# Kernel tuning notes

Measured on AMD Instinct MI355X. Metric: run time of the kernel, lower is better.

The kernel has to match this reference:

```python
import jax, jax.numpy as jnp
import numpy as np

SEQ, B, IN, H = 256, 64, 512, 1024


def setup_inputs() -> dict:
    key = jax.random.key(0)
    ks = jax.random.split(key, 17)
    s_in = 0.05  # small init to avoid gate saturation
    inp = {"x": jax.random.normal(ks[0], (SEQ, B, IN), dtype=jnp.float32)}
    names = ["f", "i", "o", "c"]
    for j, g in enumerate(names):
        inp[f"W_i{g}"] = jax.random.normal(ks[1 + 4 * j], (H, IN), dtype=jnp.float32) * s_in
        inp[f"b_i{g}"] = jax.random.normal(ks[2 + 4 * j], (H,), dtype=jnp.float32) * s_in
        inp[f"W_h{g}"] = jax.random.normal(ks[3 + 4 * j], (H, H), dtype=jnp.float32) * s_in
        inp[f"b_h{g}"] = jax.random.normal(ks[4 + 4 * j], (H,), dtype=jnp.float32) * s_in
    return inp


def reference(x, W_if, b_if, W_hf, b_hf, W_ii, b_ii, W_hi, b_hi,
              W_io, b_io, W_ho, b_ho, W_ic, b_ic, W_hc, b_hc):
    # Precompute input-to-gate projections for the whole sequence (one big GEMM each)
    xf = jnp.einsum('sbi,hi->sbh', x, W_if) + b_if
    xi = jnp.einsum('sbi,hi->sbh', x, W_ii) + b_ii
    xo = jnp.einsum('sbi,hi->sbh', x, W_io) + b_io
    xc = jnp.einsum('sbi,hi->sbh', x, W_ic) + b_ic

    batch = x.shape[1]
    hidden = W_hf.shape[0]
    h0 = jnp.zeros((batch, hidden), dtype=x.dtype)
    c0 = jnp.zeros((batch, hidden), dtype=x.dtype)

    def step(carry, xs):
        h, c = carry
        xf_t, xi_t, xo_t, xc_t = xs
        f = jax.nn.sigmoid(xf_t + h @ W_hf.T + b_hf)
        i = jax.nn.sigmoid(xi_t + h @ W_hi.T + b_hi)
        o = jax.nn.sigmoid(xo_t + h @ W_ho.T + b_ho)
        g = jnp.tanh(xc_t + h @ W_hc.T + b_hc)
        c_new = f * c + i * g
        h_new = o * jnp.tanh(c_new)
        return (h_new, c_new), h_new

    (h_fin, c_fin), h_seq = jax.lax.scan(step, (h0, c0), (xf, xi, xo, xc))
    # match torch module's (1, B, H) leading layer dim on final states
    return h_seq, h_fin[None], c_fin[None]
```

## Files before the change

kernel.cpp:

```cpp
#include <hip/hip_runtime.h>
#include <hip/hip_bf16.h>

typedef __bf16 bf16_t;
typedef __bf16 bf16x8 __attribute__((ext_vector_type(8)));
typedef float f32x4 __attribute__((ext_vector_type(4)));
typedef int   i32x4 __attribute__((ext_vector_type(4)));

#define SEQLEN 256
#define NBATCH 64
#define INDIM  512
#define HID    1024
#define NBLK   256

#define XF_OFF   0ull
#define WXF_OFF  16777216ull
#define WHF_OFF  20971520ull
#define BS_OFF   29360128ull
#define HSEQ_OFF 29376512ull
#define FLG_OFF  63062016ull
#define SLOT_BYTES 131072ull
#define SLOT_ELEMS 65536

__device__ __forceinline__ bf16x8 cvt8(float4 a, float4 b) {
  bf16x8 v;
  v[0] = (bf16_t)a.x; v[1] = (bf16_t)a.y; v[2] = (bf16_t)a.z; v[3] = (bf16_t)a.w;
  v[4] = (bf16_t)b.x; v[5] = (bf16_t)b.y; v[6] = (bf16_t)b.z; v[7] = (bf16_t)b.w;
  return v;
}

__global__ __launch_bounds__(256) void pack_xf_k(const float* __restrict__ x,
                                                 bf16_t* __restrict__ xf) {
  int idx = blockIdx.x * 256 + threadIdx.x;
  int t = idx >> 12;
  int r = idx & 4095;
  int batch = r >> 6, c8 = r & 63;
  const float4* s = (const float4*)(x + ((size_t)t * NBATCH + batch) * INDIM + c8 * 8);
  int kk = c8 >> 2, lhi = c8 & 3;
  int kh = kk >> 3, kkl = kk & 7;
  int bg = batch >> 4, lane = (batch & 15) + 16 * lhi;
  bf16_t* d = xf + (size_t)t * 32768 + (size_t)(((bg * 2 + kh) * 8 + kkl) * 64 + lane) * 8;
  *(bf16x8*)d = cvt8(s[0], s[1]);
}

struct GatePtrs {
  const float* Wi[4];
  const float* bi[4];
  const float* Wh[4];
  const float* bh[4];
};

__global__ __launch_bounds__(256) void pack_w_k(GatePtrs p,
                                                bf16_t* __restrict__ Wxf,
                                                bf16_t* __restrict__ Whf,
                                                float* __restrict__ bsum) {
  int idx = blockIdx.x * 256 + threadIdx.x;
  int row = idx / 192;
  int c   = idx % 192;
  int blk = row >> 5, r32 = row & 31, g = r32 >> 3, jj = r32 & 7;
  int j = blk * 8 + jj;
  int g2 = r32 >> 4, lrow = r32 & 15;
  if (c == 0) bsum[row] = p.bi[g][j] + p.bh[g][j];
  if (c < 64) {
    const float4* s = (const float4*)(p.Wi[g] + (size_t)j * INDIM + c * 8);
    int kk = c >> 2, lane = lrow + 16 * (c & 3);
    *(bf16x8*)(Wxf + (size_t)blk * 16384 + (size_t)((kk * 2 + g2) * 64 + lane) * 8) = cvt8(s[0], s[1]);
  } else {
    int cc = c - 64;
    const float4* s = (const float4*)(p.Wh[g] + (size_t)j * HID + cc * 8);
    int kk = cc >> 2, lane = lrow + 16 * (cc & 3);
    *(bf16x8*)(Whf + (size_t)blk * 32768 + (size_t)((kk * 2 + g2) * 64 + lane) * 8) = cvt8(s[0], s[1]);
  }
}

__global__ __launch_bounds__(256) void finalize_k(const bf16_t* __restrict__ hseq,
                                                  float* __restrict__ out) {
  int idx = blockIdx.x * 256 + threadIdx.x;
  int c = idx & 127;
  int batch = (idx >> 7) & 63;
  int t = idx >> 13;
  int slot = (t < 256) ? (t + 1) : 256;
  int j0 = c * 8;
  int kkg = j0 >> 5;
  int sub = (j0 & 31) >> 3;
  int lane = (batch & 15) + 16 * sub;
  int bg2 = (batch >> 4) * 2 + (kkg >> 4);
  const bf16_t* src = hseq + (size_t)slot * SLOT_ELEMS + (size_t)((bg2 * 16 + (kkg & 15)) * 64 + lane) * 8;
  bf16x8 v = *(const bf16x8*)src;
  float* d = out + ((size_t)t * NBATCH + batch) * HID + j0;
  *(float4*)d       = make_float4((float)v[0], (float)v[1], (float)v[2], (float)v[3]);
  *(float4*)(d + 4) = make_float4((float)v[4], (float)v[5], (float)v[6], (float)v[7]);
}

#define PLDC(dst, ptr, OFF) \
  asm volatile("global_load_dwordx4 %0, %1, off offset:" OFF : "=v"(dst) : "v"(ptr))

__global__ __launch_bounds__(256, 1) void lstm_rec_k(const bf16_t* __restrict__ Whf,
                                                     const bf16_t* __restrict__ Wxf,
                                                     const bf16_t* __restrict__ xf,
                                                     const float* __restrict__ bsum,
                                                     bf16_t* __restrict__ hseq,
                                                     int* __restrict__ flags,
                                                     float* __restrict__ out) {
  const int b = blockIdx.x;
  const int cb = b & 127, bgs = b >> 7;
  const int tid = threadIdx.x;
  const int w = tid >> 6, l = tid & 63;
  const int bhalf = w >> 1, kh = w & 1;
  const int bg = bgs * 2 + bhalf;

  __shared__ bf16_t xwlds[16384];
  __shared__ float  accbuf[2][32][36];

#pragma unroll
  for (int i = 0; i < 8; ++i)
    __builtin_amdgcn_global_load_lds((const __attribute__((address_space(1))) void*)(Wxf + (size_t)cb * 16384 + (i * 256 + tid) * 8),
                                     (__attribute__((address_space(3))) void*)(xwlds + (i * 256 + tid) * 8),
                                     16, 0, 0);

  i32x4 whr[16][2];
  {
    const char* wb = (const char*)Whf + (size_t)cb * 65536 + (size_t)(kh * 32768) + (size_t)l * 16;
    const char* w0 = wb;          const char* w1 = wb + 4096;
    const char* w2 = wb + 8192;   const char* w3 = wb + 12288;
    const char* w4 = wb + 16384;  const char* w5 = wb + 20480;
    const char* w6 = wb + 24576;  const char* w7 = wb + 28672;
    PLDC(whr[0][0],  w0, "0"); PLDC(whr[0][1],  w0, "1024"); PLDC(whr[1][0],  w0, "2048"); PLDC(whr[1][1],  w0, "3072");
    PLDC(whr[2][0],  w1, "0"); PLDC(whr[2][1],  w1, "1024"); PLDC(whr[3][0],  w1, "2048"); PLDC(whr[3][1],  w1, "3072");
    PLDC(whr[4][0],  w2, "0"); PLDC(whr[4][1],  w2, "1024"); PLDC(whr[5][0],  w2, "2048"); PLDC(whr[5][1],  w2, "3072");
    PLDC(whr[6][0],  w3, "0"); PLDC(whr[6][1],  w3, "1024"); PLDC(whr[7][0],  w3, "2048"); PLDC(whr[7][1],  w3, "3072");
    PLDC(whr[8][0],  w4, "0"); PLDC(whr[8][1],  w4, "1024"); PLDC(whr[9][0],  w4, "2048"); PLDC(whr[9][1],  w4, "3072");
    PLDC(whr[10][0], w5, "0"); PLDC(whr[10][1], w5, "1024"); PLDC(whr[11][0], w5, "2048"); PLDC(whr[11][1], w5, "3072");
    PLDC(whr[12][0], w6, "0"); PLDC(whr[12][1], w6, "1024"); PLDC(whr[13][0], w6, "2048"); PLDC(whr[13][1], w6, "3072");
    PLDC(whr[14][0], w7, "0"); PLDC(whr[14][1], w7, "1024"); PLDC(whr[15][0], w7, "2048"); PLDC(whr[15][1], w7, "3072");
  }
  asm volatile("s_waitcnt vmcnt(0)" ::: "memory");
  __builtin_amdgcn_sched_barrier(0);

  const int eb = tid >> 3, ejj = tid & 7;
  const int gb = bgs * 32 + eb;
  const int j  = cb * 8 + ejj;
  const int p_lane = (gb & 15) + 16 * ((j & 31) >> 3);
  const int p_kkg = j >> 5;
  const size_t pub_off = (size_t)((((gb >> 4) * 2 + (p_kkg >> 4)) * 16 + (p_kkg & 15)) * 64 + p_lane) * 16
                       + (size_t)(j & 7) * 2;
  const float bsF = bsum[cb * 32 + ejj];
  const float bsI = bsum[cb * 32 + 8 + ejj];
  const float bsO = bsum[cb * 32 + 16 + ejj];
  const float bsC = bsum[cb * 32 + 24 + ejj];
  float cs = 0.f;

  const size_t pollbase = (size_t)((bg * 2 + kh) * 16) * 1024 + (size_t)l * 16;
  const char* fbase = (const char*)flags + (size_t)l * 16;

  __syncthreads();

  for (int t = 0; t < SEQLEN; ++t) {
    const char* xp0 = (const char*)xf + (size_t)t * 65536 + (size_t)((bg * 2 + kh) * 8 * 64 + l) * 16;
    const char* xp1 = xp0 + 4096;
    i32x4 xr[8];
    PLDC(xr[0], xp0, "0"); PLDC(xr[1], xp0, "1024"); PLDC(xr[2], xp0, "2048"); PLDC(xr[3], xp0, "3072");
    PLDC(xr[4], xp1, "0"); PLDC(xr[5], xp1, "1024"); PLDC(xr[6], xp1, "2048"); PLDC(xr[7], xp1, "3072");
    const char* fp = fbase + (size_t)t * 1024;
    i32x4 f;
    asm volatile("global_load_dwordx4 %0, %1, off sc0 sc1" : "=v"(f) : "v"(fp));

    asm volatile("s_waitcnt vmcnt(1)" ::: "memory");
    __builtin_amdgcn_sched_barrier(0);
    f32x4 acc0 = {}, acc1 = {};
#pragma unroll
    for (int kkl = 0; kkl < 8; ++kkl) {
      const int kk = kh * 8 + kkl;
      bf16x8 xv = __builtin_bit_cast(bf16x8, xr[kkl]);
      bf16x8 w0 = *(const bf16x8*)(xwlds + (size_t)((kk * 2 + 0) * 64 + l) * 8);
      bf16x8 w1 = *(const bf16x8*)(xwlds + (size_t)((kk * 2 + 1) * 64 + l) * 8);
      acc0 = __builtin_amdgcn_mfma_f32_16x16x32_bf16(xv, w0, acc0, 0, 0, 0);
      acc1 = __builtin_amdgcn_mfma_f32_16x16x32_bf16(xv, w1, acc1, 0, 0, 0);
    }

    asm volatile("s_waitcnt vmcnt(0)" ::: "memory");
    __builtin_amdgcn_sched_barrier(0);
    while (__any((f[0] == 0) | (f[1] == 0) | (f[2] == 0) | (f[3] == 0))) {
      __builtin_amdgcn_s_sleep(1);
      asm volatile("global_load_dwordx4 %0, %1, off sc0 sc1" : "=v"(f) : "v"(fp));
      asm volatile("s_waitcnt vmcnt(0)" ::: "memory");
      __builtin_amdgcn_sched_barrier(0);
    }

    const char* q0 = (const char*)hseq + (size_t)t * SLOT_BYTES + pollbase;
    const char* q1 = q0 + 4096;
    const char* q2 = q0 + 8192;
    const char* q3 = q0 + 12288;
    i32x4 hv[16];
    PLDC(hv[0],  q0, "0"); PLDC(hv[1],  q0, "1024"); PLDC(hv[2],  q0, "2048"); PLDC(hv[3],  q0, "3072");
    PLDC(hv[4],  q1, "0"); PLDC(hv[5],  q1, "1024"); PLDC(hv[6],  q1, "2048"); PLDC(hv[7],  q1, "3072");
    PLDC(hv[8],  q2, "0"); PLDC(hv[9],  q2, "1024"); PLDC(hv[10], q2, "2048"); PLDC(hv[11], q2, "3072");
    PLDC(hv[12], q3, "0"); PLDC(hv[13], q3, "1024"); PLDC(hv[14], q3, "2048"); PLDC(hv[15], q3, "3072");
    asm volatile("s_waitcnt vmcnt(0)" ::: "memory");
    __builtin_amdgcn_sched_barrier(0);

#pragma unroll
    for (int kkl = 0; kkl < 16; ++kkl) {
      bf16x8 hf = __builtin_bit_cast(bf16x8, hv[kkl]);
      acc0 = __builtin_amdgcn_mfma_f32_16x16x32_bf16(hf, __builtin_bit_cast(bf16x8, whr[kkl][0]), acc0, 0, 0, 0);
      acc1 = __builtin_amdgcn_mfma_f32_16x16x32_bf16(hf, __builtin_bit_cast(bf16x8, whr[kkl][1]), acc1, 0, 0, 0);
    }

    *(f32x4*)&accbuf[kh][l & 15][bhalf * 16 + (l >> 4) * 4]        = acc0;
    *(f32x4*)&accbuf[kh][16 + (l & 15)][bhalf * 16 + (l >> 4) * 4] = acc1;
    __syncthreads();

    {
      float pf = bsF + accbuf[0][ejj][eb]      + accbuf[1][ejj][eb];
      float pi = bsI + accbuf[0][8 + ejj][eb]  + accbuf[1][8 + ejj][eb];
      float po = bsO + accbuf[0][16 + ejj][eb] + accbuf[1][16 + ejj][eb];
      float pc = bsC + accbuf[0][24 + ejj][eb] + accbuf[1][24 + ejj][eb];
      float fg = 1.f / (1.f + __expf(-pf));
      float ig = 1.f / (1.f + __expf(-pi));
      float og = 1.f / (1.f + __expf(-po));
      float e2 = __expf(-2.f * fabsf(pc));
      float gg = __builtin_copysignf((1.f - e2) / (1.f + e2), pc);
      cs = fg * cs + ig * gg;
      float e2c = __expf(-2.f * fabsf(cs));
      float th = __builtin_copysignf((1.f - e2c) / (1.f + e2c), cs);
      float hval = og * th;

      unsigned int my = (unsigned int)__builtin_bit_cast(unsigned short, (bf16_t)hval);
      unsigned int other = __shfl_xor(my, 1);
      if (!(tid & 1)) {
        unsigned int pk = my | (other << 16);
        unsigned int* hd = (unsigned int*)((char*)hseq + (size_t)(t + 1) * SLOT_BYTES + pub_off);
        __hip_atomic_store(hd, pk, __ATOMIC_RELAXED, __HIP_MEMORY_SCOPE_AGENT);
      }
      if (t == SEQLEN - 1)
        out[(size_t)SEQLEN * NBATCH * HID + (size_t)NBATCH * HID + (size_t)gb * HID + j] = cs;
    }

    __syncthreads();
    if (t < SEQLEN - 1 && tid == 0)
      __hip_atomic_store(&flags[(t + 1) * NBLK + b], 1, __ATOMIC_RELAXED, __HIP_MEMORY_SCOPE_AGENT);
  }
}

extern "C" void kernel_launch(void* const* d_in, const int* in_sizes, int n_in,
                              void* d_out, int out_size, void* d_ws, size_t ws_size,
                              hipStream_t stream) {
  (void)in_sizes; (void)n_in; (void)out_size; (void)ws_size;
  char* ws = (char*)d_ws;
  bf16_t* xf   = (bf16_t*)(ws + XF_OFF);
  bf16_t* Wxf  = (bf16_t*)(ws + WXF_OFF);
  bf16_t* Whf  = (bf16_t*)(ws + WHF_OFF);
  float*  bs   = (float*)(ws + BS_OFF);
  bf16_t* hseq = (bf16_t*)(ws + HSEQ_OFF);
  int*    flg  = (int*)(ws + FLG_OFF);

  const float* x = (const float*)d_in[0];
  GatePtrs p;
  for (int g = 0; g < 4; ++g) {
    p.Wi[g] = (const float*)d_in[1 + 4 * g];
    p.bi[g] = (const float*)d_in[2 + 4 * g];
    p.Wh[g] = (const float*)d_in[3 + 4 * g];
    p.bh[g] = (const float*)d_in[4 + 4 * g];
  }

  pack_xf_k<<<4096, 256, 0, stream>>>(x, xf);
  pack_w_k<<<3072, 256, 0, stream>>>(p, Wxf, Whf, bs);
  hipMemsetAsync(flg, 1, NBLK * 4, stream);
  hipMemsetAsync(flg + NBLK, 0, 256 * NBLK * 4, stream);
  hipMemsetAsync(hseq, 0, SLOT_BYTES, stream);
  lstm_rec_k<<<NBLK, 256, 0, stream>>>(Whf, Wxf, xf, bs, hseq, flg, (float*)d_out);
  finalize_k<<<8224, 256, 0, stream>>>(hseq, (float*)d_out);
}
```

Before: 749.7 us.

## Restrict flag polling to batch-group peers and prefetch next step's x and flags

Each block now waits only on the flags of the 128 blocks in its own batch group, not on all 256 blocks. The next step's x tile and flag are loaded before the block barrier, and the flag is polled right after publishing, so the x projection MFMAs overlap the h loads. The accumulators are split into even and odd chains to break MFMA dependency chains. The s_sleep in the spin loop is removed, which cuts wake-up latency but adds more memory traffic while polling.

```diff
diff --git a/kernel.cpp b/kernel.cpp
--- a/kernel.cpp
+++ b/kernel.cpp
@@ -150,42 +150,30 @@
   float cs = 0.f;
 
   const size_t pollbase = (size_t)((bg * 2 + kh) * 16) * 1024 + (size_t)l * 16;
-  const char* fbase = (const char*)flags + (size_t)l * 16;
+  const char* fbase = (const char*)flags + (size_t)bgs * 512 + (size_t)(l & 31) * 16;
 
   __syncthreads();
 
-  for (int t = 0; t < SEQLEN; ++t) {
-    const char* xp0 = (const char*)xf + (size_t)t * 65536 + (size_t)((bg * 2 + kh) * 8 * 64 + l) * 16;
+  i32x4 xr[8];
+  {
+    const char* xp0 = (const char*)xf + (size_t)((bg * 2 + kh) * 8 * 64 + l) * 16;
     const char* xp1 = xp0 + 4096;
-    i32x4 xr[8];
     PLDC(xr[0], xp0, "0"); PLDC(xr[1], xp0, "1024"); PLDC(xr[2], xp0, "2048"); PLDC(xr[3], xp0, "3072");
     PLDC(xr[4], xp1, "0"); PLDC(xr[5], xp1, "1024"); PLDC(xr[6], xp1, "2048"); PLDC(xr[7], xp1, "3072");
-    const char* fp = fbase + (size_t)t * 1024;
+  }
+  {
     i32x4 f;
-    asm volatile("global_load_dwordx4 %0, %1, off sc0 sc1" : "=v"(f) : "v"(fp));
-
-    asm volatile("s_waitcnt vmcnt(1)" ::: "memory");
-    __builtin_amdgcn_sched_barrier(0);
-    f32x4 acc0 = {}, acc1 = {};
-#pragma unroll
-    for (int kkl = 0; kkl < 8; ++kkl) {
-      const int kk = kh * 8 + kkl;
-      bf16x8 xv = __builtin_bit_cast(bf16x8, xr[kkl]);
-      bf16x8 w0 = *(const bf16x8*)(xwlds + (size_t)((kk * 2 + 0) * 64 + l) * 8);
-      bf16x8 w1 = *(const bf16x8*)(xwlds + (size_t)((kk * 2 + 1) * 64 + l) * 8);
-      acc0 = __builtin_amdgcn_mfma_f32_16x16x32_bf16(xv, w0, acc0, 0, 0, 0);
-      acc1 = __builtin_amdgcn_mfma_f32_16x16x32_bf16(xv, w1, acc1, 0, 0, 0);
-    }
-
+    asm volatile("global_load_dwordx4 %0, %1, off sc0 sc1" : "=v"(f) : "v"(fbase));
     asm volatile("s_waitcnt vmcnt(0)" ::: "memory");
     __builtin_amdgcn_sched_barrier(0);
     while (__any((f[0] == 0) | (f[1] == 0) | (f[2] == 0) | (f[3] == 0))) {
-      __builtin_amdgcn_s_sleep(1);
-      asm volatile("global_load_dwordx4 %0, %1, off sc0 sc1" : "=v"(f) : "v"(fp));
+      asm volatile("global_load_dwordx4 %0, %1, off sc0 sc1" : "=v"(f) : "v"(fbase));
       asm volatile("s_waitcnt vmcnt(0)" ::: "memory");
       __builtin_amdgcn_sched_barrier(0);
     }
-
+  }
+
+  for (int t = 0; t < SEQLEN; ++t) {
     const char* q0 = (const char*)hseq + (size_t)t * SLOT_BYTES + pollbase;
     const char* q1 = q0 + 4096;
     const char* q2 = q0 + 8192;
@@ -195,15 +183,31 @@
     PLDC(hv[4],  q1, "0"); PLDC(hv[5],  q1, "1024"); PLDC(hv[6],  q1, "2048"); PLDC(hv[7],  q1, "3072");
     PLDC(hv[8],  q2, "0"); PLDC(hv[9],  q2, "1024"); PLDC(hv[10], q2, "2048"); PLDC(hv[11], q2, "3072");
     PLDC(hv[12], q3, "0"); PLDC(hv[13], q3, "1024"); PLDC(hv[14], q3, "2048"); PLDC(hv[15], q3, "3072");
+
+    f32x4 a0e = {}, a0o = {}, a1e = {}, a1o = {};
+#pragma unroll
+    for (int kkl = 0; kkl < 8; kkl += 2) {
+      const int kk = kh * 8 + kkl;
+      bf16x8 xv0 = __builtin_bit_cast(bf16x8, xr[kkl]);
+      bf16x8 xv1 = __builtin_bit_cast(bf16x8, xr[kkl + 1]);
+      a0e = __builtin_amdgcn_mfma_f32_16x16x32_bf16(xv0, *(const bf16x8*)(xwlds + (size_t)(((kk) * 2 + 0) * 64 + l) * 8), a0e, 0, 0, 0);
+      a1e = __builtin_amdgcn_mfma_f32_16x16x32_bf16(xv0, *(const bf16x8*)(xwlds + (size_t)(((kk) * 2 + 1) * 64 + l) * 8), a1e, 0, 0, 0);
+      a0o = __builtin_amdgcn_mfma_f32_16x16x32_bf16(xv1, *(const bf16x8*)(xwlds + (size_t)(((kk + 1) * 2 + 0) * 64 + l) * 8), a0o, 0, 0, 0);
+      a1o = __builtin_amdgcn_mfma_f32_16x16x32_bf16(xv1, *(const bf16x8*)(xwlds + (size_t)(((kk + 1) * 2 + 1) * 64 + l) * 8), a1o, 0, 0, 0);
+    }
+
     asm volatile("s_waitcnt vmcnt(0)" ::: "memory");
     __builtin_amdgcn_sched_barrier(0);
-
 #pragma unroll
-    for (int kkl = 0; kkl < 16; ++kkl) {
-      bf16x8 hf = __builtin_bit_cast(bf16x8, hv[kkl]);
-      acc0 = __builtin_amdgcn_mfma_f32_16x16x32_bf16(hf, __builtin_bit_cast(bf16x8, whr[kkl][0]), acc0, 0, 0, 0);
-      acc1 = __builtin_amdgcn_mfma_f32_16x16x32_bf16(hf, __builtin_bit_cast(bf16x8, whr[kkl][1]), acc1, 0, 0, 0);
-    }
+    for (int kkl = 0; kkl < 16; kkl += 2) {
+      bf16x8 h0 = __builtin_bit_cast(bf16x8, hv[kkl]);
+      bf16x8 h1 = __builtin_bit_cast(bf16x8, hv[kkl + 1]);
+      a0e = __builtin_amdgcn_mfma_f32_16x16x32_bf16(h0, __builtin_bit_cast(bf16x8, whr[kkl][0]), a0e, 0, 0, 0);
+      a1e = __builtin_amdgcn_mfma_f32_16x16x32_bf16(h0, __builtin_bit_cast(bf16x8, whr[kkl][1]), a1e, 0, 0, 0);
+      a0o = __builtin_amdgcn_mfma_f32_16x16x32_bf16(h1, __builtin_bit_cast(bf16x8, whr[kkl + 1][0]), a0o, 0, 0, 0);
+      a1o = __builtin_amdgcn_mfma_f32_16x16x32_bf16(h1, __builtin_bit_cast(bf16x8, whr[kkl + 1][1]), a1o, 0, 0, 0);
+    }
+    f32x4 acc0 = a0e + a0o, acc1 = a1e + a1o;
 
     *(f32x4*)&accbuf[kh][l & 15][bhalf * 16 + (l >> 4) * 4]        = acc0;
     *(f32x4*)&accbuf[kh][16 + (l & 15)][bhalf * 16 + (l >> 4) * 4] = acc1;
@@ -235,9 +239,26 @@
         out[(size_t)SEQLEN * NBATCH * HID + (size_t)NBATCH * HID + (size_t)gb * HID + j] = cs;
     }
 
-    __syncthreads();
-    if (t < SEQLEN - 1 && tid == 0)
-      __hip_atomic_store(&flags[(t + 1) * NBLK + b], 1, __ATOMIC_RELAXED, __HIP_MEMORY_SCOPE_AGENT);
+    if (t < SEQLEN - 1) {
+      const char* xp0 = (const char*)xf + (size_t)(t + 1) * 65536 + (size_t)((bg * 2 + kh) * 8 * 64 + l) * 16;
+      const char* xp1 = xp0 + 4096;
+      PLDC(xr[0], xp0, "0"); PLDC(xr[1], xp0, "1024"); PLDC(xr[2], xp0, "2048"); PLDC(xr[3], xp0, "3072");
+      PLDC(xr[4], xp1, "0"); PLDC(xr[5], xp1, "1024"); PLDC(xr[6], xp1, "2048"); PLDC(xr[7], xp1, "3072");
+      const char* fp = fbase + (size_t)(t + 1) * 1024;
+      i32x4 f;
+      asm volatile("global_load_dwordx4 %0, %1, off sc0 sc1" : "=v"(f) : "v"(fp));
+      asm volatile("s_waitcnt vmcnt(0)" ::: "memory");
+      __builtin_amdgcn_sched_barrier(0);
+      __syncthreads();
+      if (tid == 0)
+        __hip_atomic_store(&flags[(t + 1) * 256 + bgs * 128 + cb], 1,
+                           __ATOMIC_RELAXED, __HIP_MEMORY_SCOPE_AGENT);
+      while (__any((f[0] == 0) | (f[1] == 0) | (f[2] == 0) | (f[3] == 0))) {
+        asm volatile("global_load_dwordx4 %0, %1, off sc0 sc1" : "=v"(f) : "v"(fp));
+        asm volatile("s_waitcnt vmcnt(0)" ::: "memory");
+        __builtin_amdgcn_sched_barrier(0);
+      }
+    }
   }
 }
 
@@ -264,8 +285,8 @@
 
   pack_xf_k<<<4096, 256, 0, stream>>>(x, xf);
   pack_w_k<<<3072, 256, 0, stream>>>(p, Wxf, Whf, bs);
-  hipMemsetAsync(flg, 1, NBLK * 4, stream);
-  hipMemsetAsync(flg + NBLK, 0, 256 * NBLK * 4, stream);
+  hipMemsetAsync(flg, 1, 256 * 4, stream);
+  hipMemsetAsync(flg + 256, 0, 256 * 256 * 4, stream);
   hipMemsetAsync(hseq, 0, SLOT_BYTES, stream);
   lstm_rec_k<<<NBLK, 256, 0, stream>>>(Whf, Wxf, xf, bs, hseq, flg, (float*)d_out);
   finalize_k<<<8224, 256, 0, stream>>>(hseq, (float*)d_out);
```

New measurement: 1.597 ms. 113% more time.
